# Optimization experiments

Measured on AMD Instinct MI355X. Metric: run time of the kernel, lower is better.

Reference implementation:

```python
import jax, jax.numpy as jnp
import numpy as np

B, N, OBS, MSG, H = 512, 128, 128, 64, 4
DH = MSG // H  # head dim = 16
ENC_HID, INT_HID = 128, 256
LN_EPS = 1e-5


def setup_inputs() -> dict:
    key = jax.random.key(0)
    ks = jax.random.split(key, 12)

    def w(k, shape):
        fan_in = shape[0]
        return (jax.random.normal(k, shape, jnp.float32) / np.sqrt(fan_in)).astype(jnp.float32)

    return {
        "obs_all": jax.random.normal(ks[0], (B, N, OBS), jnp.float32),
        # msg_encoder: Linear(obs,128) -> ReLU -> Linear(128,msg)
        "enc_w1": w(ks[1], (OBS, ENC_HID)), "enc_b1": jnp.zeros((ENC_HID,), jnp.float32),
        "enc_w2": w(ks[2], (ENC_HID, MSG)), "enc_b2": jnp.zeros((MSG,), jnp.float32),
        # MultiheadAttention in/out projections
        "wq": w(ks[3], (MSG, MSG)), "bq": jnp.zeros((MSG,), jnp.float32),
        "wk": w(ks[4], (MSG, MSG)), "bk": jnp.zeros((MSG,), jnp.float32),
        "wv": w(ks[5], (MSG, MSG)), "bv": jnp.zeros((MSG,), jnp.float32),
        "wo": w(ks[6], (MSG, MSG)), "bo": jnp.zeros((MSG,), jnp.float32),
        # integrator: Linear(obs+msg,256) -> LayerNorm -> ReLU -> Linear(256,obs)
        "int_w1": w(ks[7], (OBS + MSG, INT_HID)), "int_b1": jnp.zeros((INT_HID,), jnp.float32),
        "ln_g": jnp.ones((INT_HID,), jnp.float32), "ln_b": jnp.zeros((INT_HID,), jnp.float32),
        "int_w2": w(ks[8], (INT_HID, OBS)), "int_b2": jnp.zeros((OBS,), jnp.float32),
    }


def reference(obs_all, enc_w1, enc_b1, enc_w2, enc_b2,
              wq, bq, wk, bk, wv, bv, wo, bo,
              int_w1, int_b1, ln_g, ln_b, int_w2, int_b2):
    b, n, _ = obs_all.shape
    # send(): msg encoder MLP over all agents at once
    msgs = jnp.maximum(obs_all @ enc_w1 + enc_b1, 0.0) @ enc_w2 + enc_b2  # (B,N,MSG)

    # aggregate_messages for every agent i == full self-attention over the N agent tokens
    q = (msgs @ wq + bq).reshape(b, n, H, DH)
    k = (msgs @ wk + bk).reshape(b, n, H, DH)
    v = (msgs @ wv + bv).reshape(b, n, H, DH)
    scores = jnp.einsum('bqhd,bkhd->bhqk', q, k) / np.float32(np.sqrt(DH))
    attn = jax.nn.softmax(scores, axis=-1)
    ctx = jnp.einsum('bhqk,bkhd->bqhd', attn, v).reshape(b, n, MSG)
    agg = ctx @ wo + bo  # (B,N,MSG)

    # receive(): integrator MLP with LayerNorm
    comb = jnp.concatenate([obs_all, agg], axis=-1)  # (B,N,OBS+MSG)
    h = comb @ int_w1 + int_b1
    mu = jnp.mean(h, axis=-1, keepdims=True)
    var = jnp.mean(jnp.square(h - mu), axis=-1, keepdims=True)
    h = (h - mu) / jnp.sqrt(var + LN_EPS) * ln_g + ln_b
    h = jnp.maximum(h, 0.0)
    enriched = h @ int_w2 + int_b2  # (B,N,OBS)
    return enriched, msgs
```

## Files before the change

### kernel.cpp

```cpp
#include <hip/hip_runtime.h>
#include <math.h>

#define BB    512
#define NN    128
#define OBSD  128
#define MSGD  64
#define EHID  128
#define IHID  256

typedef __attribute__((ext_vector_type(8))) short          s16x8;
typedef __attribute__((ext_vector_type(4))) short          s16x4;
typedef __attribute__((ext_vector_type(8))) unsigned short u16x8;
typedef __attribute__((ext_vector_type(4))) unsigned short u16x4;
typedef __attribute__((ext_vector_type(4))) float          f32x4;

__device__ __forceinline__ unsigned short f2bf(float f) {
    unsigned u = __builtin_bit_cast(unsigned, f);
    return (unsigned short)((u + 0x7fffu + ((u >> 16) & 1u)) >> 16);
}
__device__ __forceinline__ float bf2f(unsigned short b) {
    return __builtin_bit_cast(float, ((unsigned)b) << 16);
}

#if defined(__has_builtin) && __has_builtin(__builtin_amdgcn_mfma_f32_16x16x16bf16_1k)
__device__ __forceinline__ f32x4 MFMA16(s16x4 a, s16x4 b, f32x4 c) {
    return __builtin_amdgcn_mfma_f32_16x16x16bf16_1k(a, b, c, 0, 0, 0);
}
#else
__device__ __forceinline__ f32x4 MFMA16(s16x4 a, s16x4 b, f32x4 c) {
    f32x4 d;
    asm volatile("v_mfma_f32_16x16x16_bf16 %0, %1, %2, %3\n\ts_nop 7\n\ts_nop 7"
                 : "=v"(d) : "v"(a), "v"(b), "v"(c));
    return d;
}
#endif

__global__ __launch_bounds__(256) void k_prep1(
    const float* __restrict__ ew2, const float* __restrict__ eb2,
    const float* __restrict__ wq, const float* __restrict__ bq,
    const float* __restrict__ wk, const float* __restrict__ bk,
    const float* __restrict__ wv, const float* __restrict__ bv,
    const float* __restrict__ wo, const float* __restrict__ bo,
    const float* __restrict__ iw1, const float* __restrict__ ib1,
    float* __restrict__ wsf)
{
    int idx = blockIdx.x * 256 + threadIdx.x;
    if (idx >= 41472) return;
    if (idx < 24576) {
        const float* W = (idx < 8192) ? wq : (idx < 16384) ? wk : wv;
        int t = idx & 8191;
        int k = t >> 6, n = t & 63;
        float s = 0.0f;
        for (int m = 0; m < 64; ++m) s = fmaf(ew2[k * 64 + m], W[m * 64 + n], s);
        wsf[idx] = s;
    } else if (idx < 40960) {
        int t = idx - 24576;
        int k = t >> 8, n = t & 255;
        float s = 0.0f;
        for (int m = 0; m < 64; ++m) s = fmaf(wo[k * 64 + m], iw1[(128 + m) * 256 + n], s);
        wsf[idx] = s;
    } else if (idx < 41216) {
        int n = idx - 40960;
        float s;
        if (n < 64) s = eb2[n];
        else {
            int c = n & 63;
            const float* W = (n < 128) ? wq : (n < 192) ? wk : wv;
            const float* bb = (n < 128) ? bq : (n < 192) ? bk : bv;
            s = bb[c];
            for (int m = 0; m < 64; ++m) s = fmaf(eb2[m], W[m * 64 + c], s);
        }
        wsf[idx] = s;
    } else {
        int n = idx - 41216;
        float s = ib1[n];
        for (int m = 0; m < 64; ++m) s = fmaf(bo[m], iw1[(128 + m) * 256 + n], s);
        wsf[idx] = s;
    }
}

__global__ __launch_bounds__(512) void k_prep2(
    const float* __restrict__ ew1, const float* __restrict__ ew2,
    const float* __restrict__ iw1, const float* __restrict__ iw2,
    const float* __restrict__ wsf, unsigned short* __restrict__ wsu)
{
    int b = blockIdx.x, t = threadIdx.x;
    int l = t >> 3, j = t & 7;
    int c = l & 15, g = l >> 4;
    float v;
    unsigned short* dst;
    if (b < 32) {
        int kk = b >> 3, nt = b & 7;
        int k = kk * 32 + g * 8 + j, n = nt * 16 + c;
        v = ew1[k * 128 + n];
        dst = wsu + b * 512;
    } else if (b < 96) {
        int tt = b - 32;
        int kk = tt >> 4, nt = tt & 15;
        int k = kk * 32 + g * 8 + j, n = nt * 16 + c;
        if (n < 64)       v = ew2[k * 64 + n];
        else if (n < 128) v = wsf[0     + k * 64 + (n - 64)];
        else if (n < 192) v = wsf[8192  + k * 64 + (n - 128)];
        else              v = wsf[16384 + k * 64 + (n - 192)];
        dst = wsu + 16384 + tt * 512;
    } else if (b < 160) {
        int tt = b - 96;
        int kk = tt >> 4, nt = tt & 15;
        int k = kk * 32 + g * 8 + j, n = nt * 16 + c;
        v = iw1[k * 256 + n];
        dst = wsu + 49152 + tt * 512;
    } else if (b < 192) {
        int tt = b - 160;
        int kk = tt >> 4, nt = tt & 15;
        int k = kk * 32 + g * 8 + j, n = nt * 16 + c;
        v = wsf[24576 + k * 256 + n];
        dst = wsu + 81920 + tt * 512;
    } else {
        int tt = b - 192;
        int kk = tt >> 3, nt = tt & 7;
        int k = kk * 32 + g * 8 + j, n = nt * 16 + c;
        v = iw2[k * 128 + n];
        dst = wsu + 98304 + tt * 512;
    }
    dst[l * 8 + j] = f2bf(v);
}

__global__ __launch_bounds__(512, 4) void k_fused(
    const float* __restrict__ obs,
    const unsigned short* __restrict__ ew1s, const float* __restrict__ eb1,
    const unsigned short* __restrict__ wcats, const float* __restrict__ bcat,
    float* __restrict__ msgs_out,
    const unsigned short* __restrict__ iw1ts, const unsigned short* __restrict__ wfs,
    const float* __restrict__ bfold, const float* __restrict__ lng,
    const float* __restrict__ lnb, const unsigned short* __restrict__ iw2s,
    const float* __restrict__ ib2, float* __restrict__ out)
{
    __shared__ unsigned short U[34816];
    __shared__ float part[128][8];

    const int tid = threadIdx.x, lane = tid & 63, w = tid >> 6;
    const int wm = w >> 2, wn = w & 3;
    const int c15 = lane & 15, grp = lane >> 4;
    const long tok0 = (long)blockIdx.x * 128;
    const f32x4 zero = {0.f, 0.f, 0.f, 0.f};

    {
        const float4* src = (const float4*)(obs + tok0 * OBSD);
        #pragma unroll
        for (int i = 0; i < 8; ++i) {
            int f = tid + i * 512;
            int t = f >> 5, kq = (f & 31) << 2;
            float4 v4 = src[f];
            u16x4 o;
            o[0] = f2bf(v4.x); o[1] = f2bf(v4.y); o[2] = f2bf(v4.z); o[3] = f2bf(v4.w);
            *(u16x4*)&U[t * 136 + kq] = o;
        }
    }
    __syncthreads();

    {
        f32x4 a1[4][2];
        #pragma unroll
        for (int m = 0; m < 4; ++m) { a1[m][0] = zero; a1[m][1] = zero; }
        #pragma unroll
        for (int kk = 0; kk < 4; ++kk) {
            s16x8 b0 = *(const s16x8*)&ew1s[(((kk << 3) + 2 * wn + 0) * 64 + lane) * 8];
            s16x8 b1 = *(const s16x8*)&ew1s[(((kk << 3) + 2 * wn + 1) * 64 + lane) * 8];
            #pragma unroll
            for (int m = 0; m < 4; ++m) {
                s16x8 a = *(const s16x8*)&U[(wm * 64 + m * 16 + c15) * 136 + kk * 32 + grp * 8];
                a1[m][0] = __builtin_amdgcn_mfma_f32_16x16x32_bf16(a, b0, a1[m][0], 0, 0, 0);
                a1[m][1] = __builtin_amdgcn_mfma_f32_16x16x32_bf16(a, b1, a1[m][1], 0, 0, 0);
            }
        }
        #pragma unroll
        for (int ntl = 0; ntl < 2; ++ntl) {
            int col = (2 * wn + ntl) * 16 + c15;
            float bias = eb1[col];
            #pragma unroll
            for (int m = 0; m < 4; ++m)
                #pragma unroll
                for (int r = 0; r < 4; ++r)
                    U[17408 + (wm * 64 + m * 16 + grp * 4 + r) * 136 + col] =
                        f2bf(fmaxf(a1[m][ntl][r] + bias, 0.f));
        }
    }
    __syncthreads();

    {
        f32x4 a2[4][4];
        #pragma unroll
        for (int m = 0; m < 4; ++m)
            #pragma unroll
            for (int n = 0; n < 4; ++n) a2[m][n] = zero;
        #pragma unroll
        for (int kk = 0; kk < 4; ++kk) {
            s16x8 b[4];
            #pragma unroll
            for (int ntl = 0; ntl < 4; ++ntl)
                b[ntl] = *(const s16x8*)&wcats[(((kk << 4) + 4 * wn + ntl) * 64 + lane) * 8];
            #pragma unroll
            for (int m = 0; m < 4; ++m) {
                s16x8 a = *(const s16x8*)&U[17408 + (wm * 64 + m * 16 + c15) * 136 + kk * 32 + grp * 8];
                #pragma unroll
                for (int ntl = 0; ntl < 4; ++ntl)
                    a2[m][ntl] = __builtin_amdgcn_mfma_f32_16x16x32_bf16(a, b[ntl], a2[m][ntl], 0, 0, 0);
            }
        }
        __syncthreads();

        #pragma unroll
        for (int ntl = 0; ntl < 4; ++ntl) {
            int lc = ntl * 16 + c15;
            float bias = bcat[wn * 64 + lc];
            #pragma unroll
            for (int m = 0; m < 4; ++m) {
                if (wn == 3) {
                    u16x4 o;
                    #pragma unroll
                    for (int r = 0; r < 4; ++r) o[r] = f2bf(a2[m][ntl][r] + bias);
                    *(u16x4*)&U[17408 + lc * 132 + wm * 64 + m * 16 + grp * 4] = o;
                } else {
                    #pragma unroll
                    for (int r = 0; r < 4; ++r) {
                        int t = wm * 64 + m * 16 + grp * 4 + r;
                        float v = a2[m][ntl][r] + bias;
                        if (wn == 0)      msgs_out[(tok0 + t) * MSGD + lc] = v;
                        else if (wn == 1) U[t * 68 + lc] = f2bf(v);
                        else              U[8704 + t * 68 + lc] = f2bf(v);
                    }
                }
            }
        }
    }
    __syncthreads();

    {
        s16x4 akf[8], avf[8];
        #pragma unroll
        for (int kt = 0; kt < 8; ++kt) {
            akf[kt] = *(const s16x4*)&U[8704 + (kt * 16 + c15) * 68 + wn * 16 + grp * 4];
            avf[kt] = *(const s16x4*)&U[17408 + (wn * 16 + c15) * 132 + kt * 16 + grp * 4];
        }
        f32x4 oacc[4];
        float il[4];
        #pragma unroll
        for (int qt = 0; qt < 4; ++qt) {
            s16x4 qf = *(const s16x4*)&U[(wm * 64 + qt * 16 + c15) * 68 + wn * 16 + grp * 4];
            f32x4 s8[8];
            #pragma unroll
            for (int kt = 0; kt < 8; ++kt) s8[kt] = MFMA16(akf[kt], qf, zero);
            float mx = -1e30f;
            #pragma unroll
            for (int kt = 0; kt < 8; ++kt)
                #pragma unroll
                for (int r = 0; r < 4; ++r) mx = fmaxf(mx, s8[kt][r]);
            mx = fmaxf(mx, __shfl_xor(mx, 16, 64));
            mx = fmaxf(mx, __shfl_xor(mx, 32, 64));
            float l = 0.f;
            #pragma unroll
            for (int kt = 0; kt < 8; ++kt)
                #pragma unroll
                for (int r = 0; r < 4; ++r) {
                    float e = __expf((s8[kt][r] - mx) * 0.25f);
                    s8[kt][r] = e;
                    l += e;
                }
            l += __shfl_xor(l, 16, 64);
            l += __shfl_xor(l, 32, 64);
            il[qt] = 1.0f / l;
            oacc[qt] = zero;
            #pragma unroll
            for (int kt = 0; kt < 8; ++kt) {
                s16x4 pb;
                #pragma unroll
                for (int r = 0; r < 4; ++r) pb[r] = (short)f2bf(s8[kt][r]);
                oacc[qt] = MFMA16(avf[kt], pb, oacc[qt]);
            }
        }
        __syncthreads();

        #pragma unroll
        for (int qt = 0; qt < 4; ++qt) {
            u16x4 o;
            #pragma unroll
            for (int r = 0; r < 4; ++r) o[r] = f2bf(oacc[qt][r] * il[qt]);
            *(u16x4*)&U[(wm * 64 + qt * 16 + c15) * 72 + wn * 16 + grp * 4] = o;
        }
    }
    __syncthreads();

    {
        f32x4 ai[4][4];
        #pragma unroll
        for (int m = 0; m < 4; ++m)
            #pragma unroll
            for (int n = 0; n < 4; ++n) ai[m][n] = zero;
        #pragma unroll
        for (int kk = 0; kk < 4; ++kk) {
            s16x8 b[4];
            #pragma unroll
            for (int ntl = 0; ntl < 4; ++ntl)
                b[ntl] = *(const s16x8*)&iw1ts[(((kk << 4) + 4 * wn + ntl) * 64 + lane) * 8];
            #pragma unroll
            for (int m = 0; m < 4; ++m) {
                const float* ap = obs + (tok0 + wm * 64 + m * 16 + c15) * OBSD + kk * 32 + grp * 8;
                float4 x0 = *(const float4*)ap;
                float4 x1 = *(const float4*)(ap + 4);
                s16x8 a;
                a[0] = f2bf(x0.x); a[1] = f2bf(x0.y); a[2] = f2bf(x0.z); a[3] = f2bf(x0.w);
                a[4] = f2bf(x1.x); a[5] = f2bf(x1.y); a[6] = f2bf(x1.z); a[7] = f2bf(x1.w);
                #pragma unroll
                for (int ntl = 0; ntl < 4; ++ntl)
                    ai[m][ntl] = __builtin_amdgcn_mfma_f32_16x16x32_bf16(a, b[ntl], ai[m][ntl], 0, 0, 0);
            }
        }
        #pragma unroll
        for (int kk = 0; kk < 2; ++kk) {
            s16x8 b[4];
            #pragma unroll
            for (int ntl = 0; ntl < 4; ++ntl)
                b[ntl] = *(const s16x8*)&wfs[(((kk << 4) + 4 * wn + ntl) * 64 + lane) * 8];
            #pragma unroll
            for (int m = 0; m < 4; ++m) {
                s16x8 a = *(const s16x8*)&U[(wm * 64 + m * 16 + c15) * 72 + kk * 32 + grp * 8];
                #pragma unroll
                for (int ntl = 0; ntl < 4; ++ntl)
                    ai[m][ntl] = __builtin_amdgcn_mfma_f32_16x16x32_bf16(a, b[ntl], ai[m][ntl], 0, 0, 0);
            }
        }

        float bias[4];
        #pragma unroll
        for (int ntl = 0; ntl < 4; ++ntl) bias[ntl] = bfold[(4 * wn + ntl) * 16 + c15];
        #pragma unroll
        for (int m = 0; m < 4; ++m) {
            #pragma unroll
            for (int r = 0; r < 4; ++r) {
                float s = 0.f, s2 = 0.f;
                #pragma unroll
                for (int ntl = 0; ntl < 4; ++ntl) {
                    float v = ai[m][ntl][r] + bias[ntl];
                    ai[m][ntl][r] = v;
                    s += v;
                    s2 = fmaf(v, v, s2);
                }
                #pragma unroll
                for (int msk = 1; msk < 16; msk <<= 1) {
                    s  += __shfl_xor(s,  msk, 64);
                    s2 += __shfl_xor(s2, msk, 64);
                }
                if (c15 == 0)
                    *(float2*)&part[wm * 64 + m * 16 + grp * 4 + r][2 * wn] = make_float2(s, s2);
            }
        }
        __syncthreads();

        if (tid < 128) {
            float4 p0 = *(const float4*)&part[tid][0];
            float4 p1 = *(const float4*)&part[tid][4];
            float s  = p0.x + p0.z + p1.x + p1.z;
            float s2 = p0.y + p0.w + p1.y + p1.w;
            float mu = s * (1.0f / IHID);
            float var = s2 * (1.0f / IHID) - mu * mu;
            *(float2*)&part[tid][0] = make_float2(mu, rsqrtf(var + 1e-5f));
        }
        __syncthreads();

        float gg[4], bb[4];
        #pragma unroll
        for (int ntl = 0; ntl < 4; ++ntl) {
            int col = (4 * wn + ntl) * 16 + c15;
            gg[ntl] = lng[col];
            bb[ntl] = lnb[col];
        }
        #pragma unroll
        for (int m = 0; m < 4; ++m)
            #pragma unroll
            for (int r = 0; r < 4; ++r) {
                int t = wm * 64 + m * 16 + grp * 4 + r;
                float2 mr = *(const float2*)&part[t][0];
                #pragma unroll
                for (int ntl = 0; ntl < 4; ++ntl) {
                    float v = fmaf((ai[m][ntl][r] - mr.x) * mr.y, gg[ntl], bb[ntl]);
                    U[t * 264 + (4 * wn + ntl) * 16 + c15] = f2bf(fmaxf(v, 0.f));
                }
            }
    }
    __syncthreads();

    {
        f32x4 a3[4][2];
        #pragma unroll
        for (int m = 0; m < 4; ++m) { a3[m][0] = zero; a3[m][1] = zero; }
        #pragma unroll
        for (int kk = 0; kk < 8; ++kk) {
            s16x8 b0 = *(const s16x8*)&iw2s[(((kk << 3) + 2 * wn + 0) * 64 + lane) * 8];
            s16x8 b1 = *(const s16x8*)&iw2s[(((kk << 3) + 2 * wn + 1) * 64 + lane) * 8];
            #pragma unroll
            for (int m = 0; m < 4; ++m) {
                s16x8 a = *(const s16x8*)&U[(wm * 64 + m * 16 + c15) * 264 + kk * 32 + grp * 8];
                a3[m][0] = __builtin_amdgcn_mfma_f32_16x16x32_bf16(a, b0, a3[m][0], 0, 0, 0);
                a3[m][1] = __builtin_amdgcn_mfma_f32_16x16x32_bf16(a, b1, a3[m][1], 0, 0, 0);
            }
        }
        #pragma unroll
        for (int ntl = 0; ntl < 2; ++ntl) {
            int col = (2 * wn + ntl) * 16 + c15;
            float bias2 = ib2[col];
            #pragma unroll
            for (int m = 0; m < 4; ++m)
                #pragma unroll
                for (int r = 0; r < 4; ++r)
                    out[(tok0 + wm * 64 + m * 16 + grp * 4 + r) * OBSD + col] =
                        a3[m][ntl][r] + bias2;
        }
    }
}

extern "C" void kernel_launch(void* const* d_in, const int* in_sizes, int n_in,
                              void* d_out, int out_size, void* d_ws, size_t ws_size,
                              hipStream_t stream)
{
    (void)in_sizes; (void)n_in; (void)out_size; (void)ws_size;

    const float* obs = (const float*)d_in[0];
    const float* ew1 = (const float*)d_in[1];
    const float* eb1 = (const float*)d_in[2];
    const float* ew2 = (const float*)d_in[3];
    const float* eb2 = (const float*)d_in[4];
    const float* wq  = (const float*)d_in[5];
    const float* bq  = (const float*)d_in[6];
    const float* wk  = (const float*)d_in[7];
    const float* bk  = (const float*)d_in[8];
    const float* wv  = (const float*)d_in[9];
    const float* bv  = (const float*)d_in[10];
    const float* wo  = (const float*)d_in[11];
    const float* bo  = (const float*)d_in[12];
    const float* iw1 = (const float*)d_in[13];
    const float* ib1 = (const float*)d_in[14];
    const float* lng = (const float*)d_in[15];
    const float* lnb = (const float*)d_in[16];
    const float* iw2 = (const float*)d_in[17];
    const float* ib2 = (const float*)d_in[18];

    float* enriched = (float*)d_out;
    float* msgs     = enriched + (size_t)BB * NN * OBSD;

    float* wsf = (float*)d_ws;
    unsigned short* wsu = (unsigned short*)(wsf + 41472);
    unsigned short* ew1s  = wsu;
    unsigned short* wcats = wsu + 16384;
    unsigned short* iw1ts = wsu + 49152;
    unsigned short* wfs   = wsu + 81920;
    unsigned short* iw2s  = wsu + 98304;

    const float* bcat  = wsf + 40960;
    const float* bfold = wsf + 41216;

    k_prep1<<<162, 256, 0, stream>>>(ew2, eb2, wq, bq, wk, bk, wv, bv,
                                     wo, bo, iw1, ib1, wsf);
    k_prep2<<<256, 512, 0, stream>>>(ew1, ew2, iw1, iw2, wsf, wsu);
    k_fused<<<BB, 512, 0, stream>>>(obs, ew1s, eb1, wcats, bcat, msgs,
                                    iw1ts, wfs, bfold, lng, lnb, iw2s, ib2,
                                    enriched);
}
```

Measured before the change: 174.3 us.

## Shrink LDS footprint by streaming obs from global and splitting integrator GEMM

Removes the initial staging of obs into shared memory and instead loads and converts it directly from global for the first encoder GEMM. It also splits the 256-wide LayerNorm output into two 128-column halves that feed the second integrator GEMM in turn, and places the LayerNorm partial sums inside the main buffer. Together these cut shared memory from about 73KB to about 52KB, aiming for more resident blocks per CU. The float-to-bf16 conversion is switched to the compiler's native __bf16 cast. The cost is extra barriers, a second global read of obs, and possibly different rounding from the native conversion.

Measured after the change: 210.7 us. +20.9%, slower.

```diff
diff --git a/kernel.cpp b/kernel.cpp
--- a/kernel.cpp
+++ b/kernel.cpp
@@ -15,11 +15,10 @@
 typedef __attribute__((ext_vector_type(4))) float          f32x4;
 
 __device__ __forceinline__ unsigned short f2bf(float f) {
-    unsigned u = __builtin_bit_cast(unsigned, f);
-    return (unsigned short)((u + 0x7fffu + ((u >> 16) & 1u)) >> 16);
+    return __builtin_bit_cast(unsigned short, (__bf16)f);
 }
 __device__ __forceinline__ float bf2f(unsigned short b) {
-    return __builtin_bit_cast(float, ((unsigned)b) << 16);
+    return (float)__builtin_bit_cast(__bf16, b);
 }
 
 #if defined(__has_builtin) && __has_builtin(__builtin_amdgcn_mfma_f32_16x16x16bf16_1k)
@@ -135,8 +134,8 @@
     const float* __restrict__ lnb, const unsigned short* __restrict__ iw2s,
     const float* __restrict__ ib2, float* __restrict__ out)
 {
-    __shared__ unsigned short U[34816];
-    __shared__ float part[128][8];
+    __shared__ unsigned short U[25856];
+    float* partp = (float*)&U[17408];
 
     const int tid = threadIdx.x, lane = tid & 63, w = tid >> 6;
     const int wm = w >> 2, wn = w & 3;
@@ -145,20 +144,6 @@
     const f32x4 zero = {0.f, 0.f, 0.f, 0.f};
 
     {
-        const float4* src = (const float4*)(obs + tok0 * OBSD);
-        #pragma unroll
-        for (int i = 0; i < 8; ++i) {
-            int f = tid + i * 512;
-            int t = f >> 5, kq = (f & 31) << 2;
-            float4 v4 = src[f];
-            u16x4 o;
-            o[0] = f2bf(v4.x); o[1] = f2bf(v4.y); o[2] = f2bf(v4.z); o[3] = f2bf(v4.w);
-            *(u16x4*)&U[t * 136 + kq] = o;
-        }
-    }
-    __syncthreads();
-
-    {
         f32x4 a1[4][2];
         #pragma unroll
         for (int m = 0; m < 4; ++m) { a1[m][0] = zero; a1[m][1] = zero; }
@@ -168,7 +153,12 @@
             s16x8 b1 = *(const s16x8*)&ew1s[(((kk << 3) + 2 * wn + 1) * 64 + lane) * 8];
             #pragma unroll
             for (int m = 0; m < 4; ++m) {
-                s16x8 a = *(const s16x8*)&U[(wm * 64 + m * 16 + c15) * 136 + kk * 32 + grp * 8];
+                const float* ap = obs + (tok0 + wm * 64 + m * 16 + c15) * OBSD + kk * 32 + grp * 8;
+                float4 x0 = *(const float4*)ap;
+                float4 x1 = *(const float4*)(ap + 4);
+                s16x8 a;
+                a[0] = f2bf(x0.x); a[1] = f2bf(x0.y); a[2] = f2bf(x0.z); a[3] = f2bf(x0.w);
+                a[4] = f2bf(x1.x); a[5] = f2bf(x1.y); a[6] = f2bf(x1.z); a[7] = f2bf(x1.w);
                 a1[m][0] = __builtin_amdgcn_mfma_f32_16x16x32_bf16(a, b0, a1[m][0], 0, 0, 0);
                 a1[m][1] = __builtin_amdgcn_mfma_f32_16x16x32_bf16(a, b1, a1[m][1], 0, 0, 0);
             }
@@ -181,7 +171,7 @@
             for (int m = 0; m < 4; ++m)
                 #pragma unroll
                 for (int r = 0; r < 4; ++r)
-                    U[17408 + (wm * 64 + m * 16 + grp * 4 + r) * 136 + col] =
+                    U[(wm * 64 + m * 16 + grp * 4 + r) * 136 + col] =
                         f2bf(fmaxf(a1[m][ntl][r] + bias, 0.f));
         }
     }
@@ -201,7 +191,7 @@
                 b[ntl] = *(const s16x8*)&wcats[(((kk << 4) + 4 * wn + ntl) * 64 + lane) * 8];
             #pragma unroll
             for (int m = 0; m < 4; ++m) {
-                s16x8 a = *(const s16x8*)&U[17408 + (wm * 64 + m * 16 + c15) * 136 + kk * 32 + grp * 8];
+                s16x8 a = *(const s16x8*)&U[(wm * 64 + m * 16 + c15) * 136 + kk * 32 + grp * 8];
                 #pragma unroll
                 for (int ntl = 0; ntl < 4; ++ntl)
                     a2[m][ntl] = __builtin_amdgcn_mfma_f32_16x16x32_bf16(a, b[ntl], a2[m][ntl], 0, 0, 0);
@@ -290,18 +280,22 @@
     }
     __syncthreads();
 
+    f32x4 ai[4][2][2];
     {
-        f32x4 ai[4][4];
         #pragma unroll
         for (int m = 0; m < 4; ++m)
             #pragma unroll
-            for (int n = 0; n < 4; ++n) ai[m][n] = zero;
+            for (int h = 0; h < 2; ++h)
+                #pragma unroll
+                for (int n = 0; n < 2; ++n) ai[m][h][n] = zero;
         #pragma unroll
         for (int kk = 0; kk < 4; ++kk) {
-            s16x8 b[4];
-            #pragma unroll
-            for (int ntl = 0; ntl < 4; ++ntl)
-                b[ntl] = *(const s16x8*)&iw1ts[(((kk << 4) + 4 * wn + ntl) * 64 + lane) * 8];
+            s16x8 b[2][2];
+            #pragma unroll
+            for (int h = 0; h < 2; ++h)
+                #pragma unroll
+                for (int ntl = 0; ntl < 2; ++ntl)
+                    b[h][ntl] = *(const s16x8*)&iw1ts[(((kk << 4) + h * 8 + 2 * wn + ntl) * 64 + lane) * 8];
             #pragma unroll
             for (int m = 0; m < 4; ++m) {
                 const float* ap = obs + (tok0 + wm * 64 + m * 16 + c15) * OBSD + kk * 32 + grp * 8;
@@ -311,66 +305,84 @@
                 a[0] = f2bf(x0.x); a[1] = f2bf(x0.y); a[2] = f2bf(x0.z); a[3] = f2bf(x0.w);
                 a[4] = f2bf(x1.x); a[5] = f2bf(x1.y); a[6] = f2bf(x1.z); a[7] = f2bf(x1.w);
                 #pragma unroll
-                for (int ntl = 0; ntl < 4; ++ntl)
-                    ai[m][ntl] = __builtin_amdgcn_mfma_f32_16x16x32_bf16(a, b[ntl], ai[m][ntl], 0, 0, 0);
+                for (int h = 0; h < 2; ++h)
+                    #pragma unroll
+                    for (int ntl = 0; ntl < 2; ++ntl)
+                        ai[m][h][ntl] = __builtin_amdgcn_mfma_f32_16x16x32_bf16(a, b[h][ntl], ai[m][h][ntl], 0, 0, 0);
             }
         }
         #pragma unroll
         for (int kk = 0; kk < 2; ++kk) {
-            s16x8 b[4];
-            #pragma unroll
-            for (int ntl = 0; ntl < 4; ++ntl)
-                b[ntl] = *(const s16x8*)&wfs[(((kk << 4) + 4 * wn + ntl) * 64 + lane) * 8];
+            s16x8 b[2][2];
+            #pragma unroll
+            for (int h = 0; h < 2; ++h)
+                #pragma unroll
+                for (int ntl = 0; ntl < 2; ++ntl)
+                    b[h][ntl] = *(const s16x8*)&wfs[(((kk << 4) + h * 8 + 2 * wn + ntl) * 64 + lane) * 8];
             #pragma unroll
             for (int m = 0; m < 4; ++m) {
                 s16x8 a = *(const s16x8*)&U[(wm * 64 + m * 16 + c15) * 72 + kk * 32 + grp * 8];
                 #pragma unroll
-                for (int ntl = 0; ntl < 4; ++ntl)
-                    ai[m][ntl] = __builtin_amdgcn_mfma_f32_16x16x32_bf16(a, b[ntl], ai[m][ntl], 0, 0, 0);
-            }
-        }
-
-        float bias[4];
-        #pragma unroll
-        for (int ntl = 0; ntl < 4; ++ntl) bias[ntl] = bfold[(4 * wn + ntl) * 16 + c15];
+                for (int h = 0; h < 2; ++h)
+                    #pragma unroll
+                    for (int ntl = 0; ntl < 2; ++ntl)
+                        ai[m][h][ntl] = __builtin_amdgcn_mfma_f32_16x16x32_bf16(a, b[h][ntl], ai[m][h][ntl], 0, 0, 0);
+            }
+        }
+
+        float bias[2][2];
+        #pragma unroll
+        for (int h = 0; h < 2; ++h)
+            #pragma unroll
+            for (int ntl = 0; ntl < 2; ++ntl)
+                bias[h][ntl] = bfold[(h * 8 + 2 * wn + ntl) * 16 + c15];
         #pragma unroll
         for (int m = 0; m < 4; ++m) {
             #pragma unroll
             for (int r = 0; r < 4; ++r) {
                 float s = 0.f, s2 = 0.f;
                 #pragma unroll
-                for (int ntl = 0; ntl < 4; ++ntl) {
-                    float v = ai[m][ntl][r] + bias[ntl];
-                    ai[m][ntl][r] = v;
-                    s += v;
-                    s2 = fmaf(v, v, s2);
-                }
+                for (int h = 0; h < 2; ++h)
+                    #pragma unroll
+                    for (int ntl = 0; ntl < 2; ++ntl) {
+                        float v = ai[m][h][ntl][r] + bias[h][ntl];
+                        ai[m][h][ntl][r] = v;
+                        s += v;
+                        s2 = fmaf(v, v, s2);
+                    }
                 #pragma unroll
                 for (int msk = 1; msk < 16; msk <<= 1) {
                     s  += __shfl_xor(s,  msk, 64);
                     s2 += __shfl_xor(s2, msk, 64);
                 }
                 if (c15 == 0)
-                    *(float2*)&part[wm * 64 + m * 16 + grp * 4 + r][2 * wn] = make_float2(s, s2);
-            }
-        }
-        __syncthreads();
-
-        if (tid < 128) {
-            float4 p0 = *(const float4*)&part[tid][0];
-            float4 p1 = *(const float4*)&part[tid][4];
-            float s  = p0.x + p0.z + p1.x + p1.z;
-            float s2 = p0.y + p0.w + p1.y + p1.w;
-            float mu = s * (1.0f / IHID);
-            float var = s2 * (1.0f / IHID) - mu * mu;
-            *(float2*)&part[tid][0] = make_float2(mu, rsqrtf(var + 1e-5f));
-        }
-        __syncthreads();
-
-        float gg[4], bb[4];
-        #pragma unroll
-        for (int ntl = 0; ntl < 4; ++ntl) {
-            int col = (4 * wn + ntl) * 16 + c15;
+                    *(float2*)&partp[(wm * 64 + m * 16 + grp * 4 + r) * 8 + 2 * wn] = make_float2(s, s2);
+            }
+        }
+    }
+    __syncthreads();
+
+    if (tid < 128) {
+        float4 p0 = *(const float4*)&partp[tid * 8];
+        float4 p1 = *(const float4*)&partp[tid * 8 + 4];
+        float s  = p0.x + p0.z + p1.x + p1.z;
+        float s2 = p0.y + p0.w + p1.y + p1.w;
+        float mu = s * (1.0f / IHID);
+        float var = s2 * (1.0f / IHID) - mu * mu;
+        *(float2*)&partp[tid * 8] = make_float2(mu, rsqrtf(var + 1e-5f));
+    }
+    __syncthreads();
+
+    f32x4 a3[4][2];
+    #pragma unroll
+    for (int m = 0; m < 4; ++m) { a3[m][0] = zero; a3[m][1] = zero; }
+
+    #pragma unroll
+    for (int h = 0; h < 2; ++h) {
+        float gg[2], bb[2];
+        #pragma unroll
+        for (int ntl = 0; ntl < 2; ++ntl) {
+            int col = (h * 8 + 2 * wn + ntl) * 16 + c15;
             gg[ntl] = lng[col];
             bb[ntl] = lnb[col];
         }
@@ -379,42 +391,40 @@
             #pragma unroll
             for (int r = 0; r < 4; ++r) {
                 int t = wm * 64 + m * 16 + grp * 4 + r;
-                float2 mr = *(const float2*)&part[t][0];
-                #pragma unroll
-                for (int ntl = 0; ntl < 4; ++ntl) {
-                    float v = fmaf((ai[m][ntl][r] - mr.x) * mr.y, gg[ntl], bb[ntl]);
-                    U[t * 264 + (4 * wn + ntl) * 16 + c15] = f2bf(fmaxf(v, 0.f));
+                float2 mr = *(const float2*)&partp[t * 8];
+                #pragma unroll
+                for (int ntl = 0; ntl < 2; ++ntl) {
+                    float v = fmaf((ai[m][h][ntl][r] - mr.x) * mr.y, gg[ntl], bb[ntl]);
+                    U[t * 136 + (2 * wn + ntl) * 16 + c15] = f2bf(fmaxf(v, 0.f));
                 }
             }
-    }
-    __syncthreads();
-
-    {
-        f32x4 a3[4][2];
-        #pragma unroll
-        for (int m = 0; m < 4; ++m) { a3[m][0] = zero; a3[m][1] = zero; }
-        #pragma unroll
-        for (int kk = 0; kk < 8; ++kk) {
-            s16x8 b0 = *(const s16x8*)&iw2s[(((kk << 3) + 2 * wn + 0) * 64 + lane) * 8];
-            s16x8 b1 = *(const s16x8*)&iw2s[(((kk << 3) + 2 * wn + 1) * 64 + lane) * 8];
-            #pragma unroll
-            for (int m = 0; m < 4; ++m) {
-                s16x8 a = *(const s16x8*)&U[(wm * 64 + m * 16 + c15) * 264 + kk * 32 + grp * 8];
+        __syncthreads();
+
+        #pragma unroll
+        for (int kk = 0; kk < 4; ++kk) {
+            int gkk = h * 4 + kk;
+            s16x8 b0 = *(const s16x8*)&iw2s[(((gkk << 3) + 2 * wn + 0) * 64 + lane) * 8];
+            s16x8 b1 = *(const s16x8*)&iw2s[(((gkk << 3) + 2 * wn + 1) * 64 + lane) * 8];
+            #pragma unroll
+            for (int m = 0; m < 4; ++m) {
+                s16x8 a = *(const s16x8*)&U[(wm * 64 + m * 16 + c15) * 136 + kk * 32 + grp * 8];
                 a3[m][0] = __builtin_amdgcn_mfma_f32_16x16x32_bf16(a, b0, a3[m][0], 0, 0, 0);
                 a3[m][1] = __builtin_amdgcn_mfma_f32_16x16x32_bf16(a, b1, a3[m][1], 0, 0, 0);
             }
         }
-        #pragma unroll
-        for (int ntl = 0; ntl < 2; ++ntl) {
-            int col = (2 * wn + ntl) * 16 + c15;
-            float bias2 = ib2[col];
-            #pragma unroll
-            for (int m = 0; m < 4; ++m)
-                #pragma unroll
-                for (int r = 0; r < 4; ++r)
-                    out[(tok0 + wm * 64 + m * 16 + grp * 4 + r) * OBSD + col] =
-                        a3[m][ntl][r] + bias2;
-        }
+        if (h == 0) __syncthreads();
+    }
+
+    #pragma unroll
+    for (int ntl = 0; ntl < 2; ++ntl) {
+        int col = (2 * wn + ntl) * 16 + c15;
+        float bias2 = ib2[col];
+        #pragma unroll
+        for (int m = 0; m < 4; ++m)
+            #pragma unroll
+            for (int r = 0; r < 4; ++r)
+                out[(tok0 + wm * 64 + m * 16 + grp * 4 + r) * OBSD + col] =
+                    a3[m][ntl][r] + bias2;
     }
 }
 
```
